# Performance work log

Hardware: AMD Instinct MI355X
Metric: run time of the kernel (lower is better)

Reference implementation:

```python
import jax, jax.numpy as jnp
import numpy as np

B, CIN, H, W = 4, 512, 63, 63
CI, CO = 256, 512  # dim_inter, dim_out
K = 9              # adaptive pool output size; H % K == 0 so pool is exact 7x7 avg
BN_EPS = 1e-5


def conv1x1(x, w, b):
    # x: [B,C,H,W], w: [O,C], b: [O]
    return jnp.einsum('bchw,oc->bohw', x, w) + b[None, :, None, None]


def bn_eval(x, gamma, beta):
    # eval-mode BatchNorm2d with running_mean=0, running_var=1
    s = gamma / jnp.sqrt(jnp.asarray(1.0 + BN_EPS, x.dtype))
    return x * s[None, :, None, None] + beta[None, :, None, None]


def setup_inputs() -> dict:
    key = jax.random.key(0)
    ks = jax.random.split(key, 11)
    sc = 0.02
    return {
        'data_input': jax.random.normal(ks[0], (B, CIN, H, W), jnp.float32),
        'Wk': jax.random.normal(ks[1], (CI, CIN), jnp.float32) * sc,
        'bk': jnp.zeros((CI,), jnp.float32),
        'gamma': 1.0 + 0.1 * jax.random.normal(ks[2], (CI,), jnp.float32),
        'beta': 0.1 * jax.random.normal(ks[3], (CI,), jnp.float32),
        'Wv': jax.random.normal(ks[4], (CI, CIN), jnp.float32) * sc,
        'bv': jnp.zeros((CI,), jnp.float32),
        'Wv2': jax.random.normal(ks[5], (CI, CI), jnp.float32) * sc,
        'bv2': jnp.zeros((CI,), jnp.float32),
        'Ww': jax.random.normal(ks[6], (CO, CI), jnp.float32) * sc,  # note: torch init is 0; randomized for a non-trivial baseline
        'bw': jnp.zeros((CO,), jnp.float32),
    }


def reference(data_input, Wk, bk, gamma, beta, Wv, bv, Wv2, bv2, Ww, bw):
    x = data_input
    scale = jnp.asarray(CI ** (-0.5), x.dtype)

    value = conv1x1(x, Wv, bv)                       # [B,CI,H,W]
    # AdaptiveAvgPool2d(9) with H,W divisible by 9 -> exact block average
    v2 = value.reshape(B, CI, K, H // K, K, W // K).mean(axis=(3, 5))  # [B,CI,9,9]
    v2 = conv1x1(v2, Wv2, bv2).reshape(B, CI, K * K)  # [B,CI,81]

    qk = bn_eval(conv1x1(x, Wk, bk), gamma, beta).reshape(B, CI, -1)  # shared query/key [B,CI,N]
    v = value.reshape(B, CI, -1)                      # [B,CI,N]

    # sim_map = softmax(Q^T K / sqrt(C)) over keys -> [B,N,N]
    sim = jax.nn.softmax(jnp.einsum('bcn,bcm->bnm', qk, qk) * scale, axis=-1)
    # sim_map_value = softmax(V^T V2 / sqrt(C)) -> [B,N,81]
    simv = jax.nn.softmax(jnp.einsum('bcn,bck->bnk', v, v2) * scale, axis=-1)

    sim_new = jnp.einsum('bnm,bmk->bnk', sim, simv)   # [B,N,81]
    ctx = jnp.einsum('bnk,bck->bcn', sim_new, v2).reshape(B, CI, H, W)
    return conv1x1(ctx, Ww, bw)                       # [B,CO,H,W]
```

## Files before the change

kernel.cpp:

```cpp
#include <hip/hip_runtime.h>
#include <hip/hip_bf16.h>

#define BB 4
#define CINsz 512
#define HH 63
#define NN 3969
#define NPAD 4032
#define NPAD2 4096
#define CI 256
#define CO 512
#define NK 81
#define NKP 96
#define SCALE 0.0625f
#define BN_EPS 1e-5f

typedef __bf16 bf16x8 __attribute__((ext_vector_type(8)));
typedef float f32x4 __attribute__((ext_vector_type(4)));
typedef unsigned short us8 __attribute__((ext_vector_type(8)));
typedef unsigned short us4 __attribute__((ext_vector_type(4)));

#define MFMA16(a, b, c) __builtin_amdgcn_mfma_f32_16x16x32_bf16((a), (b), (c), 0, 0, 0)

__device__ inline unsigned short f2bf(float x) {
    union { float f; unsigned int u; } v; v.f = x;
    unsigned int r = v.u + 0x7FFF + ((v.u >> 16) & 1);
    return (unsigned short)(r >> 16);
}
__device__ inline float bf2f(unsigned short u) {
    union { unsigned int u; float f; } v; v.u = ((unsigned int)u) << 16;
    return v.f;
}

__device__ inline void gll16(const void* g, void* l) {
    __builtin_amdgcn_global_load_lds(
        (const __attribute__((address_space(1))) unsigned int*)g,
        (__attribute__((address_space(3))) unsigned int*)l, 16, 0, 0);
}

__global__ __launch_bounds__(256) void k_prep(
    const float* __restrict__ Wk, const float* __restrict__ bk,
    const float* __restrict__ gamma, const float* __restrict__ beta,
    const float* __restrict__ Wv, const float* __restrict__ bv,
    const float* __restrict__ Wv2, const float* __restrict__ Ww,
    unsigned short* __restrict__ Wkv, float* __restrict__ bias2,
    unsigned short* __restrict__ Wv2b, unsigned short* __restrict__ Wwb,
    unsigned short* __restrict__ qkbf)
{
    int idx = blockIdx.x * 256 + threadIdx.x;
    if (idx < 512 * 512) {
        int o = idx >> 9, c = idx & 511;
        float v;
        if (o < 256) { float s = gamma[o] * rsqrtf(1.f + BN_EPS); v = Wk[(size_t)o * 512 + c] * s; }
        else v = Wv[(size_t)(o - 256) * 512 + c];
        Wkv[idx] = f2bf(v);
        if (c == 0) {
            bias2[o] = (o < 256) ? (bk[o] * (gamma[o] * rsqrtf(1.f + BN_EPS)) + beta[o]) : bv[o - 256];
        }
    } else if (idx < 512 * 512 + 256 * 256) {
        int j = idx - 512 * 512;
        Wv2b[j] = f2bf(Wv2[j]);
    } else if (idx < 512 * 512 + 256 * 256 + 512 * 256) {
        int j = idx - 512 * 512 - 256 * 256;
        Wwb[j] = f2bf(Ww[j]);
    } else if (idx < 512 * 512 + 256 * 256 + 512 * 256 + 8192) {
        int j = idx - (512 * 512 + 256 * 256 + 512 * 256);
        int b = j >> 11, rem = j & 2047;
        us8 z = (us8){0, 0, 0, 0, 0, 0, 0, 0};
        *reinterpret_cast<us8*>(&qkbf[(size_t)b * NPAD2 * CI + (size_t)NPAD * CI + rem * 8]) = z;
    }
}

__global__ __launch_bounds__(256) void k_qkv(const float* __restrict__ x,
                                             const unsigned short* __restrict__ Wkv,
                                             const float* __restrict__ bias2,
                                             unsigned short* __restrict__ qkbf,
                                             unsigned short* __restrict__ value)
{
    int b = blockIdx.y;
    int nbase = blockIdx.x * 32;
    int tid = threadIdx.x, w = tid >> 6, lane = tid & 63, lg = lane >> 4, lr = lane & 15;
    int half = w >> 1;
    int o_off = half * 256;
    int nloc = (w & 1) * 16 + lr;

    __shared__ unsigned short xs[256 * 34];
    __shared__ unsigned short wk[512 * 32];

    f32x4 acc[16];
#pragma unroll
    for (int t = 0; t < 16; ++t) acc[t] = (f32x4){0.f, 0.f, 0.f, 0.f};

    int n_l = tid & 31, cg = tid >> 5;
    int n_g = nbase + n_l;
    bool nok = n_g < NN;

    for (int h = 0; h < 2; ++h) {
        __syncthreads();
        const float* xsrc = x + ((size_t)b * CINsz + h * 256 + cg) * NN + n_g;
#pragma unroll
        for (int i = 0; i < 32; ++i) {
            int cl = cg + i * 8;
            xs[cl * 34 + n_l] = nok ? f2bf(xsrc[(size_t)(i * 8) * NN]) : (unsigned short)0;
        }
        for (int s8 = 0; s8 < 8; ++s8) {
            int c0 = (h * 8 + s8) * 32;
            __syncthreads();
#pragma unroll
            for (int j = 0; j < 8; ++j) {
                int o = w * 128 + j * 16 + (lane >> 2);
                int slot = (lane & 3) ^ (o & 3);
                gll16(Wkv + (size_t)o * CINsz + c0 + slot * 8,
                      &wk[(w * 128 + j * 16) * 32]);
            }
            __syncthreads();
            bf16x8 af;
#pragma unroll
            for (int j2 = 0; j2 < 8; ++j2)
                af[j2] = __builtin_bit_cast(__bf16, xs[(s8 * 32 + lg * 8 + j2) * 34 + nloc]);
#pragma unroll
            for (int t = 0; t < 16; ++t) {
                int o_loc = o_off + t * 16 + lr;
                bf16x8 bf = *reinterpret_cast<const bf16x8*>(
                    &wk[o_loc * 32 + ((lg ^ (o_loc & 3)) << 3)]);
                acc[t] = MFMA16(af, bf, acc[t]);
            }
        }
    }
    if (half == 0) {
        unsigned short* dst = qkbf + (size_t)b * NPAD2 * CI;
#pragma unroll
        for (int t = 0; t < 16; ++t) {
            int o = t * 16 + lr;
            float bsum = bias2[o];
#pragma unroll
            for (int r = 0; r < 4; ++r) {
                int n = nbase + (w & 1) * 16 + lg * 4 + r;
                dst[(size_t)n * CI + o] = f2bf((acc[t][r] + bsum) * 0.25f);
            }
        }
    } else {
        unsigned short* dst = value + (size_t)b * NPAD * CI;
#pragma unroll
        for (int t = 0; t < 16; ++t) {
            int o = t * 16 + lr;
            float bsum = bias2[256 + o];
#pragma unroll
            for (int r = 0; r < 4; ++r) {
                int n = nbase + (w & 1) * 16 + lg * 4 + r;
                dst[(size_t)n * CI + o] = f2bf(acc[t][r] + bsum);
            }
        }
    }
}

__global__ __launch_bounds__(256) void k_pool(const unsigned short* __restrict__ value,
                                              unsigned short* __restrict__ pooled)
{
    int b = blockIdx.y, k = blockIdx.x, c = threadIdx.x;
    unsigned short* dst = pooled + ((size_t)b * NKP + k) * CI + c;
    if (k >= NK) { *dst = 0; return; }
    int ky = k / 9, kx = k % 9;
    const unsigned short* vb = value + (size_t)b * NPAD * CI + c;
    float s = 0.f;
#pragma unroll
    for (int y = 0; y < 7; ++y)
#pragma unroll
        for (int xx = 0; xx < 7; ++xx) {
            int n = (ky * 7 + y) * HH + kx * 7 + xx;
            s += bf2f(vb[(size_t)n * CI]);
        }
    *dst = f2bf(s * (1.f / 49.f));
}

__global__ __launch_bounds__(256) void k_v2(const unsigned short* __restrict__ pooled,
                                            const unsigned short* __restrict__ Wv2b,
                                            const float* __restrict__ bv2,
                                            unsigned short* __restrict__ v2f)
{
    int b = blockIdx.y;
    int tid = threadIdx.x, w = tid >> 6, lane = tid & 63, lg = lane >> 4, lr = lane & 15;
    int ot = blockIdx.x * 4 + w;
    const unsigned short* pb = pooled + (size_t)b * NKP * CI + lg * 8;
    const unsigned short* wb = Wv2b + (size_t)(ot * 16 + lr) * CI + lg * 8;
    f32x4 acc[6];
#pragma unroll
    for (int kt = 0; kt < 6; ++kt) acc[kt] = (f32x4){0.f, 0.f, 0.f, 0.f};
#pragma unroll
    for (int s = 0; s < 8; ++s) {
        bf16x8 bfw = *reinterpret_cast<const bf16x8*>(wb + s * 32);
#pragma unroll
        for (int kt = 0; kt < 6; ++kt) {
            bf16x8 af = *reinterpret_cast<const bf16x8*>(pb + (size_t)(kt * 16 + lr) * CI + s * 32);
            acc[kt] = MFMA16(af, bfw, acc[kt]);
        }
    }
    float bias = bv2[ot * 16 + lr];
#pragma unroll
    for (int kt = 0; kt < 6; ++kt)
#pragma unroll
        for (int r = 0; r < 4; ++r)
            v2f[((size_t)b * NKP + kt * 16 + lg * 4 + r) * CI + ot * 16 + lr] = f2bf(acc[kt][r] + bias);
}

__global__ __launch_bounds__(256) void k_Z(const unsigned short* __restrict__ Wwb,
                                           const unsigned short* __restrict__ v2f,
                                           unsigned short* __restrict__ Zt)
{
    int b = blockIdx.y;
    int tid = threadIdx.x, w = tid >> 6, lane = tid & 63, lg = lane >> 4, lr = lane & 15;
    int ot = blockIdx.x * 4 + w;
    const unsigned short* wb = Wwb + (size_t)(ot * 16 + lr) * CI + lg * 8;
    const unsigned short* vb = v2f + (size_t)b * NKP * CI + lg * 8;
    f32x4 acc[6];
#pragma unroll
    for (int kt = 0; kt < 6; ++kt) acc[kt] = (f32x4){0.f, 0.f, 0.f, 0.f};
#pragma unroll
    for (int s = 0; s < 8; ++s) {
        bf16x8 af = *reinterpret_cast<const bf16x8*>(wb + s * 32);
#pragma unroll
        for (int kt = 0; kt < 6; ++kt) {
            bf16x8 bfv = *reinterpret_cast<const bf16x8*>(vb + (size_t)(kt * 16 + lr) * CI + s * 32);
            acc[kt] = MFMA16(af, bfv, acc[kt]);
        }
    }
#pragma unroll
    for (int kt = 0; kt < 6; ++kt)
#pragma unroll
        for (int r = 0; r < 4; ++r)
            Zt[((size_t)b * CO + ot * 16 + lg * 4 + r) * NKP + kt * 16 + lr] = f2bf(acc[kt][r]);
}

__global__ __launch_bounds__(256) void k_simv(const unsigned short* __restrict__ value,
                                              const unsigned short* __restrict__ v2f,
                                              unsigned short* __restrict__ svT)
{
    int b = blockIdx.y;
    int tid = threadIdx.x, w = tid >> 6, lane = tid & 63, lg = lane >> 4, lr = lane & 15;
    int n0 = blockIdx.x * 64 + w * 16;
    const unsigned short* vrow = value + ((size_t)b * NPAD + n0 + lr) * CI + lg * 8;
    const unsigned short* v2b = v2f + (size_t)b * NKP * CI + lg * 8;
    f32x4 acc[6];
#pragma unroll
    for (int kt = 0; kt < 6; ++kt) acc[kt] = (f32x4){0.f, 0.f, 0.f, 0.f};
#pragma unroll
    for (int s = 0; s < 8; ++s) {
        bf16x8 af = *reinterpret_cast<const bf16x8*>(vrow + s * 32);
#pragma unroll
        for (int kt = 0; kt < 6; ++kt) {
            bf16x8 bfv = *reinterpret_cast<const bf16x8*>(v2b + (size_t)(kt * 16 + lr) * CI + s * 32);
            acc[kt] = MFMA16(af, bfv, acc[kt]);
        }
    }
#pragma unroll
    for (int kt = 0; kt < 6; ++kt) {
        bool bad = (kt * 16 + lr) >= NK;
#pragma unroll
        for (int r = 0; r < 4; ++r) acc[kt][r] = bad ? -1e30f : acc[kt][r] * SCALE;
    }
#pragma unroll
    for (int r = 0; r < 4; ++r) {
        float m = acc[0][r];
#pragma unroll
        for (int kt = 1; kt < 6; ++kt) m = fmaxf(m, acc[kt][r]);
#pragma unroll
        for (int off = 1; off < 16; off <<= 1) m = fmaxf(m, __shfl_xor(m, off));
        float p[6], sum = 0.f;
#pragma unroll
        for (int kt = 0; kt < 6; ++kt) { p[kt] = __expf(acc[kt][r] - m); sum += p[kt]; }
#pragma unroll
        for (int off = 1; off < 16; off <<= 1) sum += __shfl_xor(sum, off);
        float inv = 1.f / sum;
#pragma unroll
        for (int kt = 0; kt < 6; ++kt) acc[kt][r] = p[kt] * inv;
    }
#pragma unroll
    for (int kt = 0; kt < 6; ++kt) {
        us4 pk;
#pragma unroll
        for (int r = 0; r < 4; ++r) pk[r] = f2bf(acc[kt][r]);
        if (kt * 16 + lr == 81) { pk[0] = pk[1] = pk[2] = pk[3] = 0x3F80; }
        *reinterpret_cast<us4*>(&svT[((size_t)b * NKP + kt * 16 + lr) * NPAD + n0 + lg * 4]) = pk;
    }
}

__global__ __launch_bounds__(256, 2) void k_flash(const unsigned short* __restrict__ qkbf,
                                                  const unsigned short* __restrict__ svT,
                                                  unsigned short* __restrict__ part_acc,
                                                  float* __restrict__ part_ml)
{
    int bid = blockIdx.x;
    int b = bid & 3;
    int rest = bid >> 2;
    int qg = rest & 31;
    int s_id = rest >> 5;
    int lo = s_id * 16;
    int hi = lo + 16 > 63 ? 63 : lo + 16;
    int tid = threadIdx.x, w = tid >> 6, lane = tid & 63, lg = lane >> 4, lr = lane & 15;
    int q0 = qg * 128 + w * 16;

    __shared__ unsigned short k_lds[2][64 * 256];
    __shared__ unsigned short sv_lds[96 * 64];

    const unsigned short* qkb = qkbf + (size_t)b * NPAD2 * CI;
    const unsigned short* svb = svT + (size_t)b * NKP * NPAD;

    bf16x8 qa[2][8];
#pragma unroll
    for (int u = 0; u < 2; ++u)
#pragma unroll
        for (int s = 0; s < 8; ++s)
            qa[u][s] = *reinterpret_cast<const bf16x8*>(
                qkb + (size_t)(q0 + u * 64 + lr) * CI + s * 32 + lg * 8);

    f32x4 acc[2][6];
#pragma unroll
    for (int u = 0; u < 2; ++u)
#pragma unroll
        for (int jt = 0; jt < 6; ++jt) acc[u][jt] = (f32x4){0.f, 0.f, 0.f, 0.f};
    float m_run[2][4];
#pragma unroll
    for (int u = 0; u < 2; ++u)
#pragma unroll
        for (int r = 0; r < 4; ++r) m_run[u][r] = -1e30f;

    auto stageK = [&](int t, int bi) {
#pragma unroll
        for (int j = 0; j < 8; ++j) {
            int r = w * 16 + j * 2 + (lane >> 5);
            int c_hw = ((lane & 31) * 8) ^ ((r & 7) << 3);
            gll16(qkb + (size_t)(t * 64 + r) * CI + c_hw,
                  &k_lds[bi][(w * 16 + j * 2) * 256]);
        }
    };
    auto stageSV = [&](int t) {
#pragma unroll
        for (int j = 0; j < 3; ++j) {
            int k = w * 24 + j * 8 + (lane >> 3);
            int m_hw = ((lane & 7) * 8) ^ ((k & 7) << 3);
            gll16(svb + (size_t)k * NPAD + t * 64 + m_hw,
                  &sv_lds[(w * 24 + j * 8) * 64]);
        }
    };

    stageK(lo, 0);
    stageSV(lo);
    __syncthreads();

    for (int t = lo; t < hi; ++t) {
        int bi = (t - lo) & 1;
        int mbase = t * 64;
        if (t + 1 < hi) stageK(t + 1, bi ^ 1);

        f32x4 s_acc[2][4];
#pragma unroll
        for (int u = 0; u < 2; ++u)
#pragma unroll
            for (int tt = 0; tt < 4; ++tt) s_acc[u][tt] = (f32x4){0.f, 0.f, 0.f, 0.f};
#pragma unroll
        for (int s = 0; s < 8; ++s) {
            bf16x8 kf[4];
#pragma unroll
            for (int tt = 0; tt < 4; ++tt) {
                int row = tt * 16 + lr;
                int hw = (s * 32 + lg * 8) ^ ((row & 7) << 3);
                kf[tt] = *reinterpret_cast<const bf16x8*>(&k_lds[bi][row * 256 + hw]);
            }
#pragma unroll
            for (int tt = 0; tt < 4; ++tt) {
                s_acc[0][tt] = MFMA16(qa[0][s], kf[tt], s_acc[0][tt]);
                s_acc[1][tt] = MFMA16(qa[1][s], kf[tt], s_acc[1][tt]);
            }
        }
        __syncthreads();

        unsigned short* pw = &k_lds[bi][w * 2048];
        bool lastTile = (mbase + 64 > NN);
#pragma unroll
        for (int u = 0; u < 2; ++u) {
            if (lastTile) {
#pragma unroll
                for (int tt = 0; tt < 4; ++tt) {
                    bool bad = (mbase + tt * 16 + lr) >= NN;
#pragma unroll
                    for (int r = 0; r < 4; ++r) if (bad) s_acc[u][tt][r] = -1e30f;
                }
            }
            float pmax[4];
#pragma unroll
            for (int r = 0; r < 4; ++r) {
                float m0 = fmaxf(fmaxf(s_acc[u][0][r], s_acc[u][1][r]),
                                 fmaxf(s_acc[u][2][r], s_acc[u][3][r]));
#pragma unroll
                for (int off = 1; off < 16; off <<= 1) m0 = fmaxf(m0, __shfl_xor(m0, off));
                pmax[r] = m0;
            }
            bool ok = (pmax[0] - m_run[u][0] <= 8.f) && (pmax[1] - m_run[u][1] <= 8.f) &&
                      (pmax[2] - m_run[u][2] <= 8.f) && (pmax[3] - m_run[u][3] <= 8.f);
            if (!__all(ok)) {
#pragma unroll
                for (int r = 0; r < 4; ++r) {
                    float mn = fmaxf(m_run[u][r], pmax[r]);
                    float al = __expf(m_run[u][r] - mn);
                    m_run[u][r] = mn;
#pragma unroll
                    for (int jt = 0; jt < 6; ++jt) acc[u][jt][r] *= al;
                }
            }
            unsigned short* pu = pw + u * 1024;
#pragma unroll
            for (int tt = 0; tt < 4; ++tt) {
#pragma unroll
                for (int r = 0; r < 4; ++r) {
                    float p = __expf(s_acc[u][tt][r] - m_run[u][r]);
                    int row = lg * 4 + r, col = tt * 16 + lr;
                    pu[row * 64 + (col ^ ((row & 7) << 3))] = f2bf(p);
                }
            }
        }
#pragma unroll
        for (int kb = 0; kb < 2; ++kb) {
            int hw = kb * 32 + lg * 8;
            int phw = hw ^ ((lr & 7) << 3);
            bf16x8 pa0 = *reinterpret_cast<const bf16x8*>(&pw[lr * 64 + phw]);
            bf16x8 pa1 = *reinterpret_cast<const bf16x8*>(&pw[1024 + lr * 64 + phw]);
#pragma unroll
            for (int jt = 0; jt < 6; ++jt) {
                int cr = jt * 16 + lr;
                bf16x8 svf = *reinterpret_cast<const bf16x8*>(
                    &sv_lds[cr * 64 + (hw ^ ((cr & 7) << 3))]);
                acc[0][jt] = MFMA16(pa0, svf, acc[0][jt]);
                acc[1][jt] = MFMA16(pa1, svf, acc[1][jt]);
            }
        }
        __syncthreads();
        if (t + 1 < hi) stageSV(t + 1);
    }
    int plane = s_id * 4 + b;
    unsigned short* pa_out = part_acc + (size_t)plane * NPAD2 * 96;
    float* ml_out = part_ml + (size_t)plane * 2 * NPAD2;
#pragma unroll
    for (int u = 0; u < 2; ++u)
#pragma unroll
        for (int r = 0; r < 4; ++r) {
            int row = q0 + u * 64 + lg * 4 + r;
#pragma unroll
            for (int jt = 0; jt < 6; ++jt)
                pa_out[(size_t)row * 96 + jt * 16 + lr] = f2bf(acc[u][jt][r]);
            if (lr == 0) ml_out[row] = m_run[u][r];
            if (lr == 1) ml_out[NPAD2 + row] = acc[u][5][r];
        }
}

__global__ __launch_bounds__(256) void k_out(const unsigned short* __restrict__ part_acc,
                                             const float* __restrict__ part_ml,
                                             const unsigned short* __restrict__ Zt,
                                             const float* __restrict__ bw,
                                             float* __restrict__ out)
{
    int b = blockIdx.z;
    int ng = blockIdx.x, og = blockIdx.y;
    int tid = threadIdx.x, w = tid >> 6, lane = tid & 63, lg = lane >> 4, lr = lane & 15;

    __shared__ unsigned short sn[64 * 104];

    for (int j = tid; j < 768; j += 256) {
        int row_l = j / 12, ch = j - row_l * 12;
        int row = ng * 64 + row_l;
        float m_s[4], l_s[4];
#pragma unroll
        for (int s = 0; s < 4; ++s) {
            const float* ml = part_ml + (size_t)(s * 4 + b) * 2 * NPAD2;
            m_s[s] = ml[row]; l_s[s] = ml[NPAD2 + row];
        }
        float mg = fmaxf(fmaxf(m_s[0], m_s[1]), fmaxf(m_s[2], m_s[3]));
        float f_s[4], denom = 0.f;
#pragma unroll
        for (int s = 0; s < 4; ++s) { f_s[s] = __expf(m_s[s] - mg); denom += f_s[s] * l_s[s]; }
        float inv = 1.f / denom;
        float a[8];
#pragma unroll
        for (int q = 0; q < 8; ++q) a[q] = 0.f;
#pragma unroll
        for (int s = 0; s < 4; ++s) {
            us8 v = *reinterpret_cast<const us8*>(
                &part_acc[((size_t)(s * 4 + b) * NPAD2 + row) * 96 + ch * 8]);
#pragma unroll
            for (int q = 0; q < 8; ++q) a[q] += f_s[s] * bf2f(v[q]);
        }
        us8 o;
#pragma unroll
        for (int q = 0; q < 8; ++q) o[q] = f2bf(a[q] * inv);
        if (ch == 10) o[1] = 0;
        *reinterpret_cast<us8*>(&sn[row_l * 104 + ch * 8]) = o;
    }
    __syncthreads();

    int o_row = (og * 4 + w) * 16;
    const unsigned short* za = Zt + ((size_t)b * CO + o_row + lr) * NKP + lg * 8;
    bf16x8 az[3];
#pragma unroll
    for (int ks = 0; ks < 3; ++ks) az[ks] = *reinterpret_cast<const bf16x8*>(za + ks * 32);
    f32x4 acc[4];
#pragma unroll
    for (int jn = 0; jn < 4; ++jn) acc[jn] = (f32x4){0.f, 0.f, 0.f, 0.f};
#pragma unroll
    for (int jn = 0; jn < 4; ++jn)
#pragma unroll
        for (int ks = 0; ks < 3; ++ks) {
            bf16x8 bfs = *reinterpret_cast<const bf16x8*>(
                &sn[(jn * 16 + lr) * 104 + ks * 32 + lg * 8]);
            acc[jn] = MFMA16(az[ks], bfs, acc[jn]);
        }
#pragma unroll
    for (int r = 0; r < 4; ++r) {
        int o = o_row + lg * 4 + r;
        float bias = bw[o];
        float* orow = out + ((size_t)b * CO + o) * NN;
#pragma unroll
        for (int jn = 0; jn < 4; ++jn) {
            int n = ng * 64 + jn * 16 + lr;
            if (n < NN) orow[n] = acc[jn][r] + bias;
        }
    }
}

extern "C" void kernel_launch(void* const* d_in, const int* in_sizes, int n_in,
                              void* d_out, int out_size, void* d_ws, size_t ws_size,
                              hipStream_t stream)
{
    const float* x     = (const float*)d_in[0];
    const float* Wk    = (const float*)d_in[1];
    const float* bk    = (const float*)d_in[2];
    const float* gamma = (const float*)d_in[3];
    const float* beta  = (const float*)d_in[4];
    const float* Wv    = (const float*)d_in[5];
    const float* bv    = (const float*)d_in[6];
    const float* Wv2   = (const float*)d_in[7];
    const float* bv2   = (const float*)d_in[8];
    const float* Ww    = (const float*)d_in[9];
    const float* bw    = (const float*)d_in[10];
    float* out = (float*)d_out;

    char* p = (char*)d_ws;
    unsigned short* qkbf   = (unsigned short*)p; p += (size_t)BB * NPAD2 * CI * 2;
    unsigned short* value  = (unsigned short*)p; p += (size_t)BB * NPAD * CI * 2;
    unsigned short* svT    = (unsigned short*)p; p += (size_t)BB * NKP * NPAD * 2;
    unsigned short* Wkv    = (unsigned short*)p; p += (size_t)512 * 512 * 2;
    unsigned short* Wv2b   = (unsigned short*)p; p += (size_t)256 * 256 * 2;
    unsigned short* Wwb    = (unsigned short*)p; p += (size_t)512 * 256 * 2;
    unsigned short* pooled = (unsigned short*)p; p += (size_t)BB * NKP * CI * 2;
    unsigned short* v2f    = (unsigned short*)p; p += (size_t)BB * NKP * CI * 2;
    unsigned short* Zt     = (unsigned short*)p; p += (size_t)BB * CO * NKP * 2;
    float* bias2           = (float*)p;          p += 512 * 4;
    unsigned short* part_acc = (unsigned short*)p; p += (size_t)16 * NPAD2 * 96 * 2;
    float* part_ml         = (float*)p;          p += (size_t)16 * 2 * NPAD2 * 4;

    k_prep<<<dim3(1826), 256, 0, stream>>>(Wk, bk, gamma, beta, Wv, bv, Wv2, Ww,
                                           Wkv, bias2, Wv2b, Wwb, qkbf);
    k_qkv<<<dim3(126, BB), 256, 0, stream>>>(x, Wkv, bias2, qkbf, value);
    k_pool<<<dim3(NKP, BB), 256, 0, stream>>>(value, pooled);
    k_v2<<<dim3(4, BB), 256, 0, stream>>>(pooled, Wv2b, bv2, v2f);
    k_Z<<<dim3(8, BB), 256, 0, stream>>>(Wwb, v2f, Zt);
    k_simv<<<dim3(63, BB), 256, 0, stream>>>(value, v2f, svT);
    k_flash<<<dim3(512), 256, 0, stream>>>(qkbf, svT, part_acc, part_ml);
    k_out<<<dim3(63, 8, BB), 256, 0, stream>>>(part_acc, part_ml, Zt, bw, out);
}
```

Measured before the change: 165.5 us.

## Halve flash key tile, double KV splits, and merge output channel groups

The flash kernel now uses 32-key tiles instead of 64, which halves its LDS footprint and allows 4 blocks per CU. Key splits grow to 8 (125 tiles), so 1024 blocks launch instead of 512. The combine/output kernel now loops over all 8 output-channel groups inside one block, so the split merge is done once per row instead of 8 times. The value buffer aliases the partial-accumulator workspace since it is dead by then. The trade-offs are more per-tile sync and softmax overhead relative to MFMA work, and larger partial buffers to merge.

```diff
diff --git a/kernel.cpp b/kernel.cpp
--- a/kernel.cpp
+++ b/kernel.cpp
@@ -13,6 +13,8 @@
 #define NKP 96
 #define SCALE 0.0625f
 #define BN_EPS 1e-5f
+#define NSPLIT 8
+#define NTILE 125
 
 typedef __bf16 bf16x8 __attribute__((ext_vector_type(8)));
 typedef float f32x4 __attribute__((ext_vector_type(4)));
@@ -283,23 +285,22 @@
     }
 }
 
-__global__ __launch_bounds__(256, 2) void k_flash(const unsigned short* __restrict__ qkbf,
+__global__ __launch_bounds__(256, 4) void k_flash(const unsigned short* __restrict__ qkbf,
                                                   const unsigned short* __restrict__ svT,
                                                   unsigned short* __restrict__ part_acc,
                                                   float* __restrict__ part_ml)
 {
     int bid = blockIdx.x;
     int b = bid & 3;
-    int rest = bid >> 2;
-    int qg = rest & 31;
-    int s_id = rest >> 5;
+    int qg = (bid >> 2) & 31;
+    int s_id = bid >> 7;
     int lo = s_id * 16;
-    int hi = lo + 16 > 63 ? 63 : lo + 16;
+    int hi = lo + 16 > NTILE ? NTILE : lo + 16;
     int tid = threadIdx.x, w = tid >> 6, lane = tid & 63, lg = lane >> 4, lr = lane & 15;
     int q0 = qg * 128 + w * 16;
 
-    __shared__ unsigned short k_lds[2][64 * 256];
-    __shared__ unsigned short sv_lds[96 * 64];
+    __shared__ unsigned short k_lds[2][32 * 256];
+    __shared__ unsigned short sv_lds[96 * 32];
 
     const unsigned short* qkb = qkbf + (size_t)b * NPAD2 * CI;
     const unsigned short* svb = svT + (size_t)b * NKP * NPAD;
@@ -325,20 +326,23 @@
 
     auto stageK = [&](int t, int bi) {
 #pragma unroll
-        for (int j = 0; j < 8; ++j) {
-            int r = w * 16 + j * 2 + (lane >> 5);
+        for (int j = 0; j < 4; ++j) {
+            int r = w * 8 + j * 2 + (lane >> 5);
             int c_hw = ((lane & 31) * 8) ^ ((r & 7) << 3);
-            gll16(qkb + (size_t)(t * 64 + r) * CI + c_hw,
-                  &k_lds[bi][(w * 16 + j * 2) * 256]);
+            gll16(qkb + (size_t)(t * 32 + r) * CI + c_hw,
+                  &k_lds[bi][(w * 8 + j * 2) * 256]);
         }
     };
     auto stageSV = [&](int t) {
 #pragma unroll
-        for (int j = 0; j < 3; ++j) {
-            int k = w * 24 + j * 8 + (lane >> 3);
-            int m_hw = ((lane & 7) * 8) ^ ((k & 7) << 3);
-            gll16(svb + (size_t)k * NPAD + t * 64 + m_hw,
-                  &sv_lds[(w * 24 + j * 8) * 64]);
+        for (int j = 0; j < 2; ++j) {
+            int L = w + j * 4;
+            if (L < 6) {
+                int k = L * 16 + (lane >> 2);
+                int slot = (lane & 3) ^ (k & 3);
+                gll16(svb + (size_t)k * NPAD + t * 32 + slot * 8,
+                      &sv_lds[L * 512]);
+            }
         }
     };
 
@@ -348,38 +352,38 @@
 
     for (int t = lo; t < hi; ++t) {
         int bi = (t - lo) & 1;
-        int mbase = t * 64;
+        int mbase = t * 32;
         if (t + 1 < hi) stageK(t + 1, bi ^ 1);
 
-        f32x4 s_acc[2][4];
+        f32x4 s_acc[2][2];
 #pragma unroll
         for (int u = 0; u < 2; ++u)
 #pragma unroll
-            for (int tt = 0; tt < 4; ++tt) s_acc[u][tt] = (f32x4){0.f, 0.f, 0.f, 0.f};
+            for (int tt = 0; tt < 2; ++tt) s_acc[u][tt] = (f32x4){0.f, 0.f, 0.f, 0.f};
 #pragma unroll
         for (int s = 0; s < 8; ++s) {
-            bf16x8 kf[4];
-#pragma unroll
-            for (int tt = 0; tt < 4; ++tt) {
+            bf16x8 kf[2];
+#pragma unroll
+            for (int tt = 0; tt < 2; ++tt) {
                 int row = tt * 16 + lr;
                 int hw = (s * 32 + lg * 8) ^ ((row & 7) << 3);
                 kf[tt] = *reinterpret_cast<const bf16x8*>(&k_lds[bi][row * 256 + hw]);
             }
 #pragma unroll
-            for (int tt = 0; tt < 4; ++tt) {
+            for (int tt = 0; tt < 2; ++tt) {
                 s_acc[0][tt] = MFMA16(qa[0][s], kf[tt], s_acc[0][tt]);
                 s_acc[1][tt] = MFMA16(qa[1][s], kf[tt], s_acc[1][tt]);
             }
         }
         __syncthreads();
 
-        unsigned short* pw = &k_lds[bi][w * 2048];
-        bool lastTile = (mbase + 64 > NN);
+        unsigned short* pw = &k_lds[bi][w * 1024];
+        bool lastTile = (mbase + 32 > NN);
 #pragma unroll
         for (int u = 0; u < 2; ++u) {
             if (lastTile) {
 #pragma unroll
-                for (int tt = 0; tt < 4; ++tt) {
+                for (int tt = 0; tt < 2; ++tt) {
                     bool bad = (mbase + tt * 16 + lr) >= NN;
 #pragma unroll
                     for (int r = 0; r < 4; ++r) if (bad) s_acc[u][tt][r] = -1e30f;
@@ -388,8 +392,7 @@
             float pmax[4];
 #pragma unroll
             for (int r = 0; r < 4; ++r) {
-                float m0 = fmaxf(fmaxf(s_acc[u][0][r], s_acc[u][1][r]),
-                                 fmaxf(s_acc[u][2][r], s_acc[u][3][r]));
+                float m0 = fmaxf(s_acc[u][0][r], s_acc[u][1][r]);
 #pragma unroll
                 for (int off = 1; off < 16; off <<= 1) m0 = fmaxf(m0, __shfl_xor(m0, off));
                 pmax[r] = m0;
@@ -406,28 +409,26 @@
                     for (int jt = 0; jt < 6; ++jt) acc[u][jt][r] *= al;
                 }
             }
-            unsigned short* pu = pw + u * 1024;
-#pragma unroll
-            for (int tt = 0; tt < 4; ++tt) {
+            unsigned short* pu = pw + u * 512;
+#pragma unroll
+            for (int tt = 0; tt < 2; ++tt) {
 #pragma unroll
                 for (int r = 0; r < 4; ++r) {
                     float p = __expf(s_acc[u][tt][r] - m_run[u][r]);
                     int row = lg * 4 + r, col = tt * 16 + lr;
-                    pu[row * 64 + (col ^ ((row & 7) << 3))] = f2bf(p);
+                    pu[row * 32 + (col ^ ((row & 3) << 3))] = f2bf(p);
                 }
             }
         }
-#pragma unroll
-        for (int kb = 0; kb < 2; ++kb) {
-            int hw = kb * 32 + lg * 8;
-            int phw = hw ^ ((lr & 7) << 3);
-            bf16x8 pa0 = *reinterpret_cast<const bf16x8*>(&pw[lr * 64 + phw]);
-            bf16x8 pa1 = *reinterpret_cast<const bf16x8*>(&pw[1024 + lr * 64 + phw]);
+        {
+            int hw = lg * 8;
+            bf16x8 pa0 = *reinterpret_cast<const bf16x8*>(&pw[lr * 32 + (hw ^ ((lr & 3) << 3))]);
+            bf16x8 pa1 = *reinterpret_cast<const bf16x8*>(&pw[512 + lr * 32 + (hw ^ ((lr & 3) << 3))]);
 #pragma unroll
             for (int jt = 0; jt < 6; ++jt) {
                 int cr = jt * 16 + lr;
                 bf16x8 svf = *reinterpret_cast<const bf16x8*>(
-                    &sv_lds[cr * 64 + (hw ^ ((cr & 7) << 3))]);
+                    &sv_lds[cr * 32 + ((lg ^ (cr & 3)) << 3)]);
                 acc[0][jt] = MFMA16(pa0, svf, acc[0][jt]);
                 acc[1][jt] = MFMA16(pa1, svf, acc[1][jt]);
             }
@@ -457,8 +458,8 @@
                                              const float* __restrict__ bw,
                                              float* __restrict__ out)
 {
-    int b = blockIdx.z;
-    int ng = blockIdx.x, og = blockIdx.y;
+    int b = blockIdx.y;
+    int ng = blockIdx.x;
     int tid = threadIdx.x, w = tid >> 6, lane = tid & 63, lg = lane >> 4, lr = lane & 15;
 
     __shared__ unsigned short sn[64 * 104];
@@ -466,22 +467,23 @@
     for (int j = tid; j < 768; j += 256) {
         int row_l = j / 12, ch = j - row_l * 12;
         int row = ng * 64 + row_l;
-        float m_s[4], l_s[4];
-#pragma unroll
-        for (int s = 0; s < 4; ++s) {
+        float m_s[NSPLIT], l_s[NSPLIT];
+        float mg = -1e30f;
+#pragma unroll
+        for (int s = 0; s < NSPLIT; ++s) {
             const float* ml = part_ml + (size_t)(s * 4 + b) * 2 * NPAD2;
             m_s[s] = ml[row]; l_s[s] = ml[NPAD2 + row];
-        }
-        float mg = fmaxf(fmaxf(m_s[0], m_s[1]), fmaxf(m_s[2], m_s[3]));
-        float f_s[4], denom = 0.f;
-#pragma unroll
-        for (int s = 0; s < 4; ++s) { f_s[s] = __expf(m_s[s] - mg); denom += f_s[s] * l_s[s]; }
+            mg = fmaxf(mg, m_s[s]);
+        }
+        float f_s[NSPLIT], denom = 0.f;
+#pragma unroll
+        for (int s = 0; s < NSPLIT; ++s) { f_s[s] = __expf(m_s[s] - mg); denom += f_s[s] * l_s[s]; }
         float inv = 1.f / denom;
         float a[8];
 #pragma unroll
         for (int q = 0; q < 8; ++q) a[q] = 0.f;
 #pragma unroll
-        for (int s = 0; s < 4; ++s) {
+        for (int s = 0; s < NSPLIT; ++s) {
             us8 v = *reinterpret_cast<const us8*>(
                 &part_acc[((size_t)(s * 4 + b) * NPAD2 + row) * 96 + ch * 8]);
 #pragma unroll
@@ -495,31 +497,33 @@
     }
     __syncthreads();
 
-    int o_row = (og * 4 + w) * 16;
-    const unsigned short* za = Zt + ((size_t)b * CO + o_row + lr) * NKP + lg * 8;
-    bf16x8 az[3];
-#pragma unroll
-    for (int ks = 0; ks < 3; ++ks) az[ks] = *reinterpret_cast<const bf16x8*>(za + ks * 32);
-    f32x4 acc[4];
-#pragma unroll
-    for (int jn = 0; jn < 4; ++jn) acc[jn] = (f32x4){0.f, 0.f, 0.f, 0.f};
-#pragma unroll
-    for (int jn = 0; jn < 4; ++jn)
-#pragma unroll
-        for (int ks = 0; ks < 3; ++ks) {
-            bf16x8 bfs = *reinterpret_cast<const bf16x8*>(
-                &sn[(jn * 16 + lr) * 104 + ks * 32 + lg * 8]);
-            acc[jn] = MFMA16(az[ks], bfs, acc[jn]);
-        }
-#pragma unroll
-    for (int r = 0; r < 4; ++r) {
-        int o = o_row + lg * 4 + r;
-        float bias = bw[o];
-        float* orow = out + ((size_t)b * CO + o) * NN;
-#pragma unroll
-        for (int jn = 0; jn < 4; ++jn) {
-            int n = ng * 64 + jn * 16 + lr;
-            if (n < NN) orow[n] = acc[jn][r] + bias;
+    for (int og = 0; og < 8; ++og) {
+        int o_row = (og * 4 + w) * 16;
+        const unsigned short* za = Zt + ((size_t)b * CO + o_row + lr) * NKP + lg * 8;
+        bf16x8 az[3];
+#pragma unroll
+        for (int ks = 0; ks < 3; ++ks) az[ks] = *reinterpret_cast<const bf16x8*>(za + ks * 32);
+        f32x4 acc[4];
+#pragma unroll
+        for (int jn = 0; jn < 4; ++jn) acc[jn] = (f32x4){0.f, 0.f, 0.f, 0.f};
+#pragma unroll
+        for (int jn = 0; jn < 4; ++jn)
+#pragma unroll
+            for (int ks = 0; ks < 3; ++ks) {
+                bf16x8 bfs = *reinterpret_cast<const bf16x8*>(
+                    &sn[(jn * 16 + lr) * 104 + ks * 32 + lg * 8]);
+                acc[jn] = MFMA16(az[ks], bfs, acc[jn]);
+            }
+#pragma unroll
+        for (int r = 0; r < 4; ++r) {
+            int o = o_row + lg * 4 + r;
+            float bias = bw[o];
+            float* orow = out + ((size_t)b * CO + o) * NN;
+#pragma unroll
+            for (int jn = 0; jn < 4; ++jn) {
+                int n = ng * 64 + jn * 16 + lr;
+                if (n < NN) orow[n] = acc[jn][r] + bias;
+            }
         }
     }
 }
@@ -543,7 +547,6 @@
 
     char* p = (char*)d_ws;
     unsigned short* qkbf   = (unsigned short*)p; p += (size_t)BB * NPAD2 * CI * 2;
-    unsigned short* value  = (unsigned short*)p; p += (size_t)BB * NPAD * CI * 2;
     unsigned short* svT    = (unsigned short*)p; p += (size_t)BB * NKP * NPAD * 2;
     unsigned short* Wkv    = (unsigned short*)p; p += (size_t)512 * 512 * 2;
     unsigned short* Wv2b   = (unsigned short*)p; p += (size_t)256 * 256 * 2;
@@ -552,8 +555,9 @@
     unsigned short* v2f    = (unsigned short*)p; p += (size_t)BB * NKP * CI * 2;
     unsigned short* Zt     = (unsigned short*)p; p += (size_t)BB * CO * NKP * 2;
     float* bias2           = (float*)p;          p += 512 * 4;
-    unsigned short* part_acc = (unsigned short*)p; p += (size_t)16 * NPAD2 * 96 * 2;
-    float* part_ml         = (float*)p;          p += (size_t)16 * 2 * NPAD2 * 4;
+    unsigned short* value    = (unsigned short*)p;
+    unsigned short* part_acc = (unsigned short*)p; p += (size_t)NSPLIT * 4 * NPAD2 * 96 * 2;
+    float* part_ml           = (float*)p;          p += (size_t)NSPLIT * 4 * 2 * NPAD2 * 4;
 
     k_prep<<<dim3(1826), 256, 0, stream>>>(Wk, bk, gamma, beta, Wv, bv, Wv2, Ww,
                                            Wkv, bias2, Wv2b, Wwb, qkbf);
@@ -562,6 +566,6 @@
     k_v2<<<dim3(4, BB), 256, 0, stream>>>(pooled, Wv2b, bv2, v2f);
     k_Z<<<dim3(8, BB), 256, 0, stream>>>(Wwb, v2f, Zt);
     k_simv<<<dim3(63, BB), 256, 0, stream>>>(value, v2f, svT);
-    k_flash<<<dim3(512), 256, 0, stream>>>(qkbf, svT, part_acc, part_ml);
-    k_out<<<dim3(63, 8, BB), 256, 0, stream>>>(part_acc, part_ml, Zt, bw, out);
-}
+    k_flash<<<dim3(1024), 256, 0, stream>>>(qkbf, svT, part_acc, part_ml);
+    k_out<<<dim3(63, BB), 256, 0, stream>>>(part_acc, part_ml, Zt, bw, out);
+}
```

New measurement: 271.8 us. 64.2% more time.
